# Performance work log

Hardware: AMD Instinct MI355X
Metric: run time of the kernel (lower is better)

The kernel has to match this reference:

```python
import jax, jax.numpy as jnp
import numpy as np

D_MODEL = 512
NHEAD = 8
D_HEAD = D_MODEL // NHEAD
SCALE = D_HEAD ** -0.5
EPS = 1e-8


def setup_inputs() -> dict:
    key = jax.random.key(0)
    ks = jax.random.split(key, 12)
    B, N = 4, 2048
    s = D_MODEL ** -0.5
    return {
        "Q_input": jax.random.normal(ks[0], (B, N, D_MODEL), jnp.float32),
        "KV_input": jax.random.normal(ks[1], (B, N, D_MODEL), jnp.float32),
        "SC": jax.random.uniform(ks[2], (B, N, N), jnp.float32),
        "Wq_w": jax.random.normal(ks[3], (D_MODEL, D_MODEL), jnp.float32) * s,
        "Wq_b": jnp.zeros((D_MODEL,), jnp.float32),
        "Wk_w": jax.random.normal(ks[4], (D_MODEL, D_MODEL), jnp.float32) * s,
        "Wk_b": jnp.zeros((D_MODEL,), jnp.float32),
        "Wv_w": jax.random.normal(ks[5], (D_MODEL, D_MODEL), jnp.float32) * s,
        "Wv_b": jnp.zeros((D_MODEL,), jnp.float32),
        "gate_w": jax.random.normal(ks[6], (), jnp.float32),
        "gate_b": jnp.zeros((), jnp.float32),
        "out_w": jax.random.normal(ks[7], (D_MODEL, D_MODEL), jnp.float32) * s,
        "out_b": jnp.zeros((D_MODEL,), jnp.float32),
    }


def reference(Q_input, KV_input, SC, Wq_w, Wq_b, Wk_w, Wk_b, Wv_w, Wv_b,
              gate_w, gate_b, out_w, out_b):
    B, N, _ = Q_input.shape
    # projections -> [B, H, N, d_head]
    def proj(x, w, b):
        y = x @ w.T + b
        return y.reshape(B, N, NHEAD, D_HEAD).transpose(0, 2, 1, 3)
    Q = proj(Q_input, Wq_w, Wq_b)
    K = proj(KV_input, Wk_w, Wk_b)
    V = proj(KV_input, Wv_w, Wv_b)
    # scores [B, H, N, N]
    scores = jnp.einsum('bhqd,bhkd->bhqk', Q, K) * SCALE
    # per-edge gate: sigmoid(w*SC + b), broadcast over heads
    g = jax.nn.sigmoid(SC * gate_w + gate_b)  # [B, N, N]
    scores = scores + jnp.log(g + EPS)[:, None, :, :]
    attn = jax.nn.softmax(scores, axis=-1)
    out = jnp.einsum('bhqk,bhkd->bhqd', attn, V)
    out = out.transpose(0, 2, 1, 3).reshape(B, N, D_MODEL)
    return out @ out_w.T + out_b
```

## Files before the change

### kernel.cpp

```cpp
#include <hip/hip_runtime.h>

typedef unsigned short u16;
typedef unsigned int u32;
typedef __attribute__((ext_vector_type(4))) float f32x4;
typedef __attribute__((ext_vector_type(8))) short s16x8;
typedef __attribute__((ext_vector_type(4))) u16 u16x4;

#define L2E 1.4426950408889634f
#define QSCALE 0.18033688011112042f

__device__ __forceinline__ float bf2f(u16 u) {
    union { u32 i; float f; } v; v.i = ((u32)u) << 16; return v.f;
}
__device__ __forceinline__ u16 f2bf(float f) {
    union { float f; u32 i; } v; v.f = f;
    return (u16)((v.i + 0x7fffu + ((v.i >> 16) & 1u)) >> 16);
}
__device__ __forceinline__ u16 f2bf_rn(float f) {
    union { float f; u32 i; } v; v.f = f;
    return (u16)((v.i + 0x8000u) >> 16);
}

__device__ __forceinline__ void gl2lds16(const u16* g, u16* l) {
    __builtin_amdgcn_global_load_lds(
        (const __attribute__((address_space(1))) void*)g,
        (__attribute__((address_space(3))) void*)l, 16, 0, 0);
}

__global__ __launch_bounds__(256) void conv_kernel(
    const float* __restrict__ s0, const float* __restrict__ s1,
    const float* __restrict__ s2, const float* __restrict__ s3,
    const float* __restrict__ s4, const float* __restrict__ s5,
    u16* __restrict__ dst)
{
    int e = (blockIdx.x * 256 + threadIdx.x) * 4;
    const float* src; int off;
    if      (e < 4194304) { src = s0; off = e; }
    else if (e < 8388608) { src = s1; off = e - 4194304; }
    else if (e < 8650752) { src = s2; off = e - 8388608; }
    else if (e < 8912896) { src = s3; off = e - 8650752; }
    else if (e < 9175040) { src = s4; off = e - 8912896; }
    else                  { src = s5; off = e - 9175040; }
    f32x4 f = *(const f32x4*)(src + off);
    u16x4 o;
#pragma unroll
    for (int j = 0; j < 4; ++j) o[j] = f2bf(f[j]);
    *(u16x4*)(dst + e) = o;
}

__global__ __launch_bounds__(256) void lg_kernel(
    const float* __restrict__ SC, const float* __restrict__ gwp,
    const float* __restrict__ gbp, u16* __restrict__ LG)
{
    int i = (blockIdx.x * 256 + threadIdx.x) * 4;
    const float tA = -gwp[0] * L2E, tB = -gbp[0] * L2E;
    f32x4 x = *(const f32x4*)(SC + i);
    u16x4 o;
#pragma unroll
    for (int j = 0; j < 4; ++j) {
        float g = __builtin_amdgcn_rcpf(
                      1.0f + __builtin_amdgcn_exp2f(tA * x[j] + tB)) + 1e-8f;
        o[j] = f2bf(__builtin_amdgcn_logf(g));
    }
    *(u16x4*)(LG + i) = o;
}

__device__ __forceinline__ void gemm_core(
    const u16* __restrict__ A, const u16* __restrict__ Bw,
    int m0, int n0, u16* As, u16* Bs, f32x4 acc[4][4])
{
    const int tid = threadIdx.x;
    const int lane = tid & 63, w = tid >> 6;
    const int wm = w >> 1, wn = w & 1;
    const int l16 = lane & 15, quad = lane >> 4;
    const int srow = (lane >> 2), sch = (lane & 3) * 8;
    const f32x4 vzero = {0.f, 0.f, 0.f, 0.f};
#pragma unroll
    for (int i = 0; i < 4; ++i)
#pragma unroll
        for (int j = 0; j < 4; ++j) acc[i][j] = vzero;

    for (int kt = 0; kt < 16; ++kt) {
#pragma unroll
        for (int j = 0; j < 2; ++j) {
            int row = w * 32 + j * 16 + srow;
            gl2lds16(&A[(size_t)(m0 + row) * 512 + kt * 32 + sch],
                     &As[w * 1024 + j * 512]);
            gl2lds16(&Bw[(size_t)(n0 + row) * 512 + kt * 32 + sch],
                     &Bs[w * 1024 + j * 512]);
        }
        __syncthreads();
        s16x8 af[4], bfr[4];
#pragma unroll
        for (int mt = 0; mt < 4; ++mt)
            af[mt] = *(const s16x8*)&As[(wm * 64 + mt * 16 + l16) * 32 + quad * 8];
#pragma unroll
        for (int nt = 0; nt < 4; ++nt)
            bfr[nt] = *(const s16x8*)&Bs[(wn * 64 + nt * 16 + l16) * 32 + quad * 8];
#pragma unroll
        for (int mt = 0; mt < 4; ++mt)
#pragma unroll
            for (int nt = 0; nt < 4; ++nt)
                acc[mt][nt] = __builtin_amdgcn_mfma_f32_16x16x32_bf16(
                    af[mt], bfr[nt], acc[mt][nt], 0, 0, 0);
        __syncthreads();
    }
}

__global__ __launch_bounds__(256) void proj_kernel(
    const u16* __restrict__ cQin, const u16* __restrict__ cKV,
    const u16* __restrict__ cW,
    const float* __restrict__ bq, const float* __restrict__ bk,
    const float* __restrict__ bv,
    u16* __restrict__ Qh, u16* __restrict__ Kh, u16* __restrict__ Vt)
{
    __shared__ __align__(16) u16 As[128 * 32];
    __shared__ __align__(16) u16 Bs[128 * 32];
    const int job = blockIdx.z;
    const u16* A = (job == 0) ? cQin : cKV;
    const u16* W = cW + (size_t)job * 262144;
    const float* bias = (job == 0) ? bq : (job == 1 ? bk : bv);
    const int m0 = blockIdx.y * 128, n0 = blockIdx.x * 128;
    f32x4 acc[4][4];
    gemm_core(A, W, m0, n0, As, Bs, acc);

    const int tid = threadIdx.x, lane = tid & 63, w = tid >> 6;
    const int wm = w >> 1, wn = w & 1, l16 = lane & 15, quad = lane >> 4;
#pragma unroll
    for (int nt = 0; nt < 4; ++nt) {
        int j = n0 + wn * 64 + nt * 16 + l16;
        float bj = bias[j];
        int h = j >> 6, d = j & 63;
#pragma unroll
        for (int mt = 0; mt < 4; ++mt) {
            int trow = m0 + wm * 64 + mt * 16 + quad * 4;
            int bb = trow >> 11, nn = trow & 2047;
            int bh = bb * 8 + h;
            if (job == 2) {
                u16x4 pv;
#pragma unroll
                for (int reg = 0; reg < 4; ++reg) pv[reg] = f2bf(acc[mt][nt][reg] + bj);
                *(u16x4*)&Vt[(size_t)(bh * 64 + d) * 2048 + nn] = pv;
            } else if (job == 0) {
#pragma unroll
                for (int reg = 0; reg < 4; ++reg)
                    Qh[(size_t)(bh * 2048 + nn + reg) * 64 + d] =
                        f2bf((acc[mt][nt][reg] + bj) * QSCALE);
            } else {
#pragma unroll
                for (int reg = 0; reg < 4; ++reg)
                    Kh[(size_t)(bh * 2048 + nn + reg) * 64 + d] =
                        f2bf(acc[mt][nt][reg] + bj);
            }
        }
    }
}

__global__ __launch_bounds__(1024, 4) void attn_kernel(
    const u16* __restrict__ Qh, const u16* __restrict__ Kh,
    const u16* __restrict__ Vt, const u16* __restrict__ LG,
    u16* __restrict__ Ob)
{
    __shared__ __align__(16) u16 Ks[2][4096];
    __shared__ __align__(16) u16 Vs[2][4096];
    __shared__ __align__(16) u16 Plds[16][16][68];
    const int tid = threadIdx.x;
    const int w = tid >> 6, lane = tid & 63;
    const int l16 = lane & 15, quad = lane >> 4;
    const int b = blockIdx.z, head = blockIdx.y;
    const int bh = b * 8 + head;
    const int q0 = blockIdx.x * 256 + w * 16;
    const u16* Qp = Qh + (size_t)bh * 131072;
    const u16* Kp = Kh + (size_t)bh * 131072;
    const u16* Vp = Vt + (size_t)bh * 131072;
    const u16* LGp = LG + (size_t)b * 4194304 + (size_t)(q0 + l16) * 2048;
    const f32x4 vzero = {0.f, 0.f, 0.f, 0.f};

    const int sr = lane >> 3;
    const int sc = ((lane & 7) ^ (sr & 7)) * 8;
    const int slab = (w & 7) * 8;
    const u16* sK = Kp + (size_t)(slab + sr) * 64 + sc;
    const u16* sV = Vp + (size_t)(slab + sr) * 2048 + sc;

    s16x8 qf[2];
#pragma unroll
    for (int kc = 0; kc < 2; ++kc)
        qf[kc] = *(const s16x8*)&Qp[(size_t)(q0 + l16) * 64 + kc * 32 + quad * 8];
    f32x4 o[4];
    float lsum = 0.f;
#pragma unroll
    for (int dn = 0; dn < 4; ++dn) o[dn] = vzero;

    if (w < 8) gl2lds16(sK, &Ks[0][slab * 64]);
    else       gl2lds16(sV, &Vs[0][slab * 64]);

    for (int kt = 0; kt < 32; ++kt) {
        __syncthreads();
        const int cur = kt & 1;
        if (kt < 31) {
            if (w < 8) gl2lds16(sK + (size_t)(kt + 1) * 4096, &Ks[cur ^ 1][slab * 64]);
            else       gl2lds16(sV + (size_t)(kt + 1) * 64,   &Vs[cur ^ 1][slab * 64]);
        }
        const u16* Kb = Ks[cur];
        const u16* Vb = Vs[cur];
        const int k0 = kt * 64;

        f32x4 st[4];
#pragma unroll
        for (int kc = 0; kc < 2; ++kc) {
            s16x8 kf[4];
#pragma unroll
            for (int kk = 0; kk < 4; ++kk)
                kf[kk] = *(const s16x8*)&Kb[(kk * 16 + l16) * 64 +
                                            ((kc * 4 + quad) ^ (l16 & 7)) * 8];
#pragma unroll
            for (int kk = 0; kk < 4; ++kk)
                st[kk] = __builtin_amdgcn_mfma_f32_16x16x32_bf16(
                    kf[kk], qf[kc], kc == 0 ? vzero : st[kk], 0, 0, 0);
        }
#pragma unroll
        for (int kk = 0; kk < 4; ++kk) {
            u16x4 lg4 = *(const u16x4*)&LGp[k0 + kk * 16 + quad * 4];
            u16x4 pp;
#pragma unroll
            for (int reg = 0; reg < 4; ++reg) {
                float p = __builtin_amdgcn_exp2f(st[kk][reg] + bf2f(lg4[reg]));
                lsum += p;
                pp[reg] = f2bf_rn(p);
            }
            *(u16x4*)&Plds[w][l16][kk * 16 + quad * 4] = pp;
        }
#pragma unroll
        for (int kc = 0; kc < 2; ++kc) {
            s16x8 pf = *(const s16x8*)&Plds[w][l16][kc * 32 + quad * 8];
            s16x8 vf[4];
#pragma unroll
            for (int dn = 0; dn < 4; ++dn)
                vf[dn] = *(const s16x8*)&Vb[(dn * 16 + l16) * 64 +
                                            ((kc * 4 + quad) ^ (l16 & 7)) * 8];
#pragma unroll
            for (int dn = 0; dn < 4; ++dn)
                o[dn] = __builtin_amdgcn_mfma_f32_16x16x32_bf16(
                    pf, vf[dn], o[dn], 0, 0, 0);
        }
    }
    lsum += __shfl_xor(lsum, 16, 64);
    lsum += __shfl_xor(lsum, 32, 64);
    float inv = __builtin_amdgcn_rcpf(lsum);
#pragma unroll
    for (int reg = 0; reg < 4; ++reg) {
        float invr = __shfl(inv, quad * 4 + reg, 64);
        int trow = b * 2048 + q0 + quad * 4 + reg;
#pragma unroll
        for (int dn = 0; dn < 4; ++dn)
            Ob[(size_t)trow * 512 + head * 64 + dn * 16 + l16] =
                f2bf(o[dn][reg] * invr);
    }
}

__global__ __launch_bounds__(256) void out_kernel(
    const u16* __restrict__ Ob, const u16* __restrict__ cWo,
    const float* __restrict__ bo, float* __restrict__ out)
{
    __shared__ __align__(16) u16 As[128 * 32];
    __shared__ __align__(16) u16 Bs[128 * 32];
    const int m0 = blockIdx.y * 128, n0 = blockIdx.x * 128;
    f32x4 acc[4][4];
    gemm_core(Ob, cWo, m0, n0, As, Bs, acc);
    const int tid = threadIdx.x, lane = tid & 63, w = tid >> 6;
    const int wm = w >> 1, wn = w & 1, l16 = lane & 15, quad = lane >> 4;
#pragma unroll
    for (int nt = 0; nt < 4; ++nt) {
        int j = n0 + wn * 64 + nt * 16 + l16;
        float bj = bo[j];
#pragma unroll
        for (int mt = 0; mt < 4; ++mt) {
            int t = m0 + wm * 64 + mt * 16 + quad * 4;
#pragma unroll
            for (int reg = 0; reg < 4; ++reg)
                out[(size_t)(t + reg) * 512 + j] = acc[mt][nt][reg] + bj;
        }
    }
}

extern "C" void kernel_launch(void* const* d_in, const int* in_sizes, int n_in,
                              void* d_out, int out_size, void* d_ws, size_t ws_size,
                              hipStream_t stream)
{
    const float* Qin  = (const float*)d_in[0];
    const float* KVin = (const float*)d_in[1];
    const float* SC   = (const float*)d_in[2];
    const float* Wq   = (const float*)d_in[3];
    const float* bq   = (const float*)d_in[4];
    const float* Wk   = (const float*)d_in[5];
    const float* bk   = (const float*)d_in[6];
    const float* Wv   = (const float*)d_in[7];
    const float* bv   = (const float*)d_in[8];
    const float* gw   = (const float*)d_in[9];
    const float* gb   = (const float*)d_in[10];
    const float* Wo   = (const float*)d_in[11];
    const float* bo   = (const float*)d_in[12];
    float* out = (float*)d_out;

    u16* conv = (u16*)d_ws;
    u16* cQin = conv;
    u16* cKV  = conv + 4194304;
    u16* cW   = conv + 8388608;
    u16* Qh   = conv + 9437184;
    u16* Kh   = Qh + 4194304;
    u16* Vt   = Kh + 4194304;
    u16* Ob   = Vt + 4194304;
    u16* LG   = Ob + 4194304;

    hipLaunchKernelGGL(conv_kernel, dim3(9216), dim3(256), 0, stream,
                       Qin, KVin, Wq, Wk, Wv, Wo, conv);
    hipLaunchKernelGGL(lg_kernel, dim3(16384), dim3(256), 0, stream,
                       SC, gw, gb, LG);
    hipLaunchKernelGGL(proj_kernel, dim3(4, 64, 3), dim3(256), 0, stream,
                       cQin, cKV, cW, bq, bk, bv, Qh, Kh, Vt);
    hipLaunchKernelGGL(attn_kernel, dim3(8, 8, 4), dim3(1024), 0, stream,
                       Qh, Kh, Vt, LG, Ob);
    hipLaunchKernelGGL(out_kernel, dim3(4, 64), dim3(256), 0, stream,
                       Ob, cW + 786432, bo, out);
}
```

Measured before the change: 283.8 us.

## Pre-swizzle log-gate tensor into MFMA fragment order and halve attention block size

The log-gate kernel now writes its output in the exact per-lane fragment order the attention kernel consumes, so each lane reads 32 contiguous bytes per key tile instead of four scattered 8-byte loads from a row-major layout. The attention kernel also moves from 1024-thread to 512-thread blocks covering 128 queries, with each wave issuing two K/V LDS staging loads. This should improve coalescing of the large LG read and change occupancy and scheduling granularity. In exchange, the lg kernel's SC reads become strided per lane, and K/V tiles are loaded twice as often across the grid.

```diff
diff --git a/kernel.cpp b/kernel.cpp
--- a/kernel.cpp
+++ b/kernel.cpp
@@ -50,19 +50,31 @@
 
 __global__ __launch_bounds__(256) void lg_kernel(
     const float* __restrict__ SC, const float* __restrict__ gwp,
-    const float* __restrict__ gbp, u16* __restrict__ LG)
-{
-    int i = (blockIdx.x * 256 + threadIdx.x) * 4;
+    const float* __restrict__ gbp, u16* __restrict__ LGx)
+{
+    const int flat = blockIdx.x * 256 + threadIdx.x;
+    const int lane = flat & 63;
+    const int kt   = (flat >> 6) & 31;
+    const int t16  = (flat >> 11) & 127;
+    const int b    = flat >> 18;
+    const int l16 = lane & 15, quad = lane >> 4;
     const float tA = -gwp[0] * L2E, tB = -gbp[0] * L2E;
-    f32x4 x = *(const f32x4*)(SC + i);
-    u16x4 o;
-#pragma unroll
-    for (int j = 0; j < 4; ++j) {
-        float g = __builtin_amdgcn_rcpf(
-                      1.0f + __builtin_amdgcn_exp2f(tA * x[j] + tB)) + 1e-8f;
-        o[j] = f2bf(__builtin_amdgcn_logf(g));
-    }
-    *(u16x4*)(LG + i) = o;
+    const float* row = SC + ((size_t)b * 2048 + t16 * 16 + l16) * 2048
+                          + kt * 64 + quad * 4;
+    __align__(16) u16 tmp[16];
+#pragma unroll
+    for (int kk = 0; kk < 4; ++kk) {
+        f32x4 x = *(const f32x4*)(row + kk * 16);
+#pragma unroll
+        for (int reg = 0; reg < 4; ++reg) {
+            float g = __builtin_amdgcn_rcpf(
+                1.0f + __builtin_amdgcn_exp2f(tA * x[reg] + tB)) + 1e-8f;
+            tmp[kk * 4 + reg] = f2bf(__builtin_amdgcn_logf(g));
+        }
+    }
+    u16* dst = LGx + (size_t)flat * 16;
+    *(uint4*)dst       = *(uint4*)tmp;
+    *(uint4*)(dst + 8) = *(uint4*)(tmp + 8);
 }
 
 __device__ __forceinline__ void gemm_core(
@@ -156,31 +168,38 @@
     }
 }
 
-__global__ __launch_bounds__(1024, 4) void attn_kernel(
+__global__ __launch_bounds__(512, 4) void attn_kernel(
     const u16* __restrict__ Qh, const u16* __restrict__ Kh,
-    const u16* __restrict__ Vt, const u16* __restrict__ LG,
+    const u16* __restrict__ Vt, const u16* __restrict__ LGx,
     u16* __restrict__ Ob)
 {
     __shared__ __align__(16) u16 Ks[2][4096];
     __shared__ __align__(16) u16 Vs[2][4096];
-    __shared__ __align__(16) u16 Plds[16][16][68];
+    __shared__ __align__(16) u16 Plds[8][16][68];
     const int tid = threadIdx.x;
     const int w = tid >> 6, lane = tid & 63;
     const int l16 = lane & 15, quad = lane >> 4;
-    const int b = blockIdx.z, head = blockIdx.y;
+    const int b = blockIdx.z, head = blockIdx.y, qg = blockIdx.x;
     const int bh = b * 8 + head;
-    const int q0 = blockIdx.x * 256 + w * 16;
+    const int q0 = qg * 128 + w * 16;
+    const int t16 = qg * 8 + w;
     const u16* Qp = Qh + (size_t)bh * 131072;
     const u16* Kp = Kh + (size_t)bh * 131072;
     const u16* Vp = Vt + (size_t)bh * 131072;
-    const u16* LGp = LG + (size_t)b * 4194304 + (size_t)(q0 + l16) * 2048;
+    const u16* LGt = LGx + ((size_t)((b * 128 + t16) * 32) * 64 + lane) * 16;
     const f32x4 vzero = {0.f, 0.f, 0.f, 0.f};
 
     const int sr = lane >> 3;
-    const int sc = ((lane & 7) ^ (sr & 7)) * 8;
-    const int slab = (w & 7) * 8;
-    const u16* sK = Kp + (size_t)(slab + sr) * 64 + sc;
-    const u16* sV = Vp + (size_t)(slab + sr) * 2048 + sc;
+    const int scw = ((lane & 7) ^ sr) * 8;
+    const int slab = (w & 3) * 16;
+    const bool isK = (w < 4);
+    const u16* sG0 = isK ? (Kp + (size_t)(slab + sr) * 64 + scw)
+                         : (Vp + (size_t)(slab + sr) * 2048 + scw);
+    const u16* sG1 = isK ? (Kp + (size_t)(slab + 8 + sr) * 64 + scw)
+                         : (Vp + (size_t)(slab + 8 + sr) * 2048 + scw);
+    const size_t sAdv = isK ? 4096 : 64;
+    u16* sL0 = isK ? &Ks[0][slab * 64] : &Vs[0][slab * 64];
+    u16* sL1 = isK ? &Ks[0][(slab + 8) * 64] : &Vs[0][(slab + 8) * 64];
 
     s16x8 qf[2];
 #pragma unroll
@@ -191,19 +210,22 @@
 #pragma unroll
     for (int dn = 0; dn < 4; ++dn) o[dn] = vzero;
 
-    if (w < 8) gl2lds16(sK, &Ks[0][slab * 64]);
-    else       gl2lds16(sV, &Vs[0][slab * 64]);
+    gl2lds16(sG0, sL0);
+    gl2lds16(sG1, sL1);
 
     for (int kt = 0; kt < 32; ++kt) {
         __syncthreads();
         const int cur = kt & 1;
         if (kt < 31) {
-            if (w < 8) gl2lds16(sK + (size_t)(kt + 1) * 4096, &Ks[cur ^ 1][slab * 64]);
-            else       gl2lds16(sV + (size_t)(kt + 1) * 64,   &Vs[cur ^ 1][slab * 64]);
-        }
-        const u16* Kb = Ks[cur];
-        const u16* Vb = Vs[cur];
-        const int k0 = kt * 64;
+            const int nxt = cur ^ 1;
+            gl2lds16(sG0 + (size_t)(kt + 1) * sAdv, sL0 + nxt * 4096);
+            gl2lds16(sG1 + (size_t)(kt + 1) * sAdv, sL1 + nxt * 4096);
+        }
+        const u16* Kb = &Ks[cur][0];
+        const u16* Vb = &Vs[cur][0];
+        __align__(16) u16 lgv[16];
+        *(uint4*)lgv       = *(const uint4*)(LGt + (size_t)kt * 1024);
+        *(uint4*)(lgv + 8) = *(const uint4*)(LGt + (size_t)kt * 1024 + 8);
 
         f32x4 st[4];
 #pragma unroll
@@ -220,11 +242,11 @@
         }
 #pragma unroll
         for (int kk = 0; kk < 4; ++kk) {
-            u16x4 lg4 = *(const u16x4*)&LGp[k0 + kk * 16 + quad * 4];
             u16x4 pp;
 #pragma unroll
             for (int reg = 0; reg < 4; ++reg) {
-                float p = __builtin_amdgcn_exp2f(st[kk][reg] + bf2f(lg4[reg]));
+                float p = __builtin_amdgcn_exp2f(st[kk][reg] +
+                                                 bf2f(lgv[kk * 4 + reg]));
                 lsum += p;
                 pp[reg] = f2bf_rn(p);
             }
@@ -310,16 +332,16 @@
     u16* Kh   = Qh + 4194304;
     u16* Vt   = Kh + 4194304;
     u16* Ob   = Vt + 4194304;
-    u16* LG   = Ob + 4194304;
+    u16* LGx  = Ob + 4194304;
 
     hipLaunchKernelGGL(conv_kernel, dim3(9216), dim3(256), 0, stream,
                        Qin, KVin, Wq, Wk, Wv, Wo, conv);
-    hipLaunchKernelGGL(lg_kernel, dim3(16384), dim3(256), 0, stream,
-                       SC, gw, gb, LG);
+    hipLaunchKernelGGL(lg_kernel, dim3(4096), dim3(256), 0, stream,
+                       SC, gw, gb, LGx);
     hipLaunchKernelGGL(proj_kernel, dim3(4, 64, 3), dim3(256), 0, stream,
                        cQin, cKV, cW, bq, bk, bv, Qh, Kh, Vt);
-    hipLaunchKernelGGL(attn_kernel, dim3(8, 8, 4), dim3(1024), 0, stream,
-                       Qh, Kh, Vt, LG, Ob);
+    hipLaunchKernelGGL(attn_kernel, dim3(16, 8, 4), dim3(512), 0, stream,
+                       Qh, Kh, Vt, LGx, Ob);
     hipLaunchKernelGGL(out_kernel, dim3(4, 64), dim3(256), 0, stream,
                        Ob, cW + 786432, bo, out);
 }
```

New measurement: 261.9 us. -7.7%, faster.
